# Performance work log

Measured on AMD Instinct MI355X. Metric: run time of the kernel, lower is better.

The kernel has to match this reference:

```python
import jax, jax.numpy as jnp
import numpy as np

D_K = 64
N_HEADS = 16
D_MODEL = 1024


def setup_inputs() -> dict:
    key = jax.random.key(0)
    ks = jax.random.split(key, 12)
    N, T = 2, 2048
    H = D_K * N_HEADS
    s = 1.0 / np.sqrt(D_MODEL)
    inp = {
        "q": jax.random.normal(ks[0], (N, T, D_MODEL), jnp.float32),
        "k": jax.random.normal(ks[1], (N, T, D_MODEL), jnp.float32),
        "v": jax.random.normal(ks[2], (N, T, D_MODEL), jnp.float32),
        "mask": jax.random.randint(ks[3], (N, T), 0, 2, jnp.int32),
        "Wq": jax.random.normal(ks[4], (D_MODEL, H), jnp.float32) * s,
        "bq": jax.random.normal(ks[5], (H,), jnp.float32) * 0.02,
        "Wk": jax.random.normal(ks[6], (D_MODEL, H), jnp.float32) * s,
        "bk": jax.random.normal(ks[7], (H,), jnp.float32) * 0.02,
        "Wv": jax.random.normal(ks[8], (D_MODEL, H), jnp.float32) * s,
        "bv": jax.random.normal(ks[9], (H,), jnp.float32) * 0.02,
        "Wo": jax.random.normal(ks[10], (H, D_MODEL), jnp.float32) * (1.0 / np.sqrt(H)),
        "bo": jax.random.normal(ks[11], (D_MODEL,), jnp.float32) * 0.02,
    }
    return inp


def reference(q, k, v, mask, Wq, bq, Wk, bk, Wv, bv, Wo, bo):
    N, T, _ = q.shape
    # project and split heads: [N, T, H*dk] -> [N, nH, T, dk]
    def split(x):
        return x.reshape(N, T, N_HEADS, D_K).transpose(0, 2, 1, 3)
    qh = split(q @ Wq + bq)
    kh = split(k @ Wk + bk)
    vh = split(v @ Wv + bv)
    scores = jnp.einsum("bhqd,bhkd->bhqk", qh, kh) / np.sqrt(D_K)
    # key padding mask: mask[:, None, None, :] == 0 -> -inf
    scores = jnp.where(mask[:, None, None, :] == 0, -jnp.inf, scores)
    attn = jax.nn.softmax(scores, axis=-1)
    A = jnp.einsum("bhqk,bhkd->bhqd", attn, vh)
    A = A.transpose(0, 2, 1, 3).reshape(N, T, N_HEADS * D_K)
    return A @ Wo + bo
```

## Files before the change

kernel.cpp:

```cpp
#include <hip/hip_runtime.h>

#define T_SEQ 2048
#define DM 1024
#define NH 16
#define DKH 64
#define NB 2
#define M_ROWS (NB * T_SEQ)
#define QSCALE 0.18033688011112042f

using bf16x8 = __attribute__((ext_vector_type(8))) __bf16;
using f32x4  = __attribute__((ext_vector_type(4))) float;
using halfx4 = __attribute__((ext_vector_type(4))) __fp16;
using halfx8 = __attribute__((ext_vector_type(8))) __fp16;
using halfx2 = __attribute__((ext_vector_type(2))) __fp16;
using uintx4 = __attribute__((ext_vector_type(4))) unsigned;

__device__ __forceinline__ short f2bf(float f) {
  unsigned u = __builtin_bit_cast(unsigned, f);
  u += 0x7fffu + ((u >> 16) & 1u);
  return (short)(u >> 16);
}

#if defined(__has_builtin) && __has_builtin(__builtin_amdgcn_cvt_pk_bf16_f32)
using bf16x2 = __attribute__((ext_vector_type(2))) __bf16;
__device__ __forceinline__ short2 pk2(float a, float b) {
  bf16x2 r = __builtin_amdgcn_cvt_pk_bf16_f32(a, b);
  return __builtin_bit_cast(short2, r);
}
#else
__device__ __forceinline__ short2 pk2(float a, float b) {
  short2 r; r.x = f2bf(a); r.y = f2bf(b); return r;
}
#endif

__device__ __forceinline__ short2 pkh(float a, float b) {
  halfx2 r = __builtin_amdgcn_cvt_pkrtz(a, b);
  return __builtin_bit_cast(short2, r);
}

#if defined(__has_builtin) && __has_builtin(__builtin_amdgcn_exp2f)
__device__ __forceinline__ float fexp2(float x) { return __builtin_amdgcn_exp2f(x); }
#else
__device__ __forceinline__ float fexp2(float x) { return exp2f(x); }
#endif

#if defined(__has_builtin) && __has_builtin(__builtin_amdgcn_permlane32_swap) && \
    __has_builtin(__builtin_amdgcn_permlane16_swap)
using uintx2 = __attribute__((ext_vector_type(2))) unsigned;
__device__ __forceinline__ void swap32(unsigned& a, unsigned& b) {
  uintx2 r = __builtin_amdgcn_permlane32_swap(a, b, false, false);
  a = r.x; b = r.y;
}
__device__ __forceinline__ void swap16(unsigned& a, unsigned& b) {
  uintx2 r = __builtin_amdgcn_permlane16_swap(a, b, false, false);
  a = r.x; b = r.y;
}
#else
__device__ __forceinline__ void swap32(unsigned& a, unsigned& b) {
  asm volatile("v_permlane32_swap_b32 %0, %1" : "+v"(a), "+v"(b));
}
__device__ __forceinline__ void swap16(unsigned& a, unsigned& b) {
  asm volatile("v_permlane16_swap_b32 %0, %1" : "+v"(a), "+v"(b));
}
#endif

#define GLD16(g, l)                                                            \
  __builtin_amdgcn_global_load_lds(                                            \
      (const __attribute__((address_space(1))) void*)(g),                      \
      (__attribute__((address_space(3))) void*)(l), 16, 0, 0)

__global__ __launch_bounds__(256) void prep_x(
    const float* __restrict__ q, const float* __restrict__ k,
    const float* __restrict__ v, const int* __restrict__ mask,
    short* __restrict__ dst, float* __restrict__ mf) {
  const float* s = blockIdx.z == 0 ? q : (blockIdx.z == 1 ? k : v);
  short* d = dst + (size_t)blockIdx.z * (M_ROWS * DM);
  const int n4 = M_ROWS * DM / 4;
  for (int i = blockIdx.x * 256 + threadIdx.x; i < n4; i += gridDim.x * 256) {
    float4 f = *(const float4*)(s + i * 4);
    short2 a = pk2(f.x, f.y), b = pk2(f.z, f.w);
    short4 o = {a.x, a.y, b.x, b.y};
    *(short4*)(d + i * 4) = o;
  }
  if (blockIdx.z == 0 && blockIdx.x < 4) {
    int i = (blockIdx.x * 256 + threadIdx.x) * 4;
    int4 m = *(const int4*)(mask + i);
    float4 o = {m.x ? 0.f : -1e38f, m.y ? 0.f : -1e38f,
                m.z ? 0.f : -1e38f, m.w ? 0.f : -1e38f};
    *(float4*)(mf + i) = o;
  }
}

__global__ __launch_bounds__(256) void prep_w(
    const float* __restrict__ w0, const float* __restrict__ w1,
    const float* __restrict__ w2, const float* __restrict__ w3,
    short* __restrict__ dst) {
  __shared__ short T[64][72];
  const float* W = blockIdx.z == 0 ? w0 : blockIdx.z == 1 ? w1
                   : blockIdx.z == 2 ? w2 : w3;
  short* D = dst + (size_t)blockIdx.z * (DM * DM);
  const int k0 = blockIdx.x * 64, n0 = blockIdx.y * 64;
  const int r = threadIdx.x >> 2, cs = (threadIdx.x & 3) * 16;
#pragma unroll
  for (int j = 0; j < 4; ++j) {
    float4 f = *(const float4*)(W + (size_t)(k0 + r) * DM + n0 + cs + j * 4);
    short2 a = pk2(f.x, f.y), b = pk2(f.z, f.w);
    short4 o = {a.x, a.y, b.x, b.y};
    *(short4*)&T[r][cs + j * 4] = o;
  }
  __syncthreads();
  short tmp[16];
#pragma unroll
  for (int i = 0; i < 16; ++i) tmp[i] = T[cs + i][r];
  *(int4*)(D + (size_t)(n0 + r) * DM + k0 + cs) = *(const int4*)&tmp[0];
  *(int4*)(D + (size_t)(n0 + r) * DM + k0 + cs + 8) = *(const int4*)&tmp[8];
}

__global__ __launch_bounds__(512) void gemm_qkv(
    const short* __restrict__ A_, const short* __restrict__ Bt_,
    const float* __restrict__ b0, const float* __restrict__ b1,
    const float* __restrict__ b2, short* __restrict__ Y) {
  __shared__ short As[2][4096];
  __shared__ short Bs[2][4096];
  const int z = blockIdx.z;
  const short* A = A_ + (size_t)z * (M_ROWS * DM);
  const short* Bt = Bt_ + (size_t)z * (DM * DM);
  short* Yz = Y + (size_t)z * ((size_t)M_ROWS * DM);
  const float* bias = z == 0 ? b0 : (z == 1 ? b1 : b2);
  const int m0 = blockIdx.x * 128, n0 = blockIdx.y * 128;
  const int tid = threadIdx.x, w = tid >> 6, lane = tid & 63;
  const int quad = lane >> 4, lm = lane & 15, wa = w & 1, wb = w >> 1;

  const short* Ag = A + (size_t)(m0 + w * 16 + lm) * DM + quad * 8;
  const short* Bg = Bt + (size_t)(n0 + w * 16 + lm) * DM + quad * 8;

  f32x4 acc[4][2];
#pragma unroll
  for (int i = 0; i < 4; ++i)
#pragma unroll
    for (int j = 0; j < 2; ++j) acc[i][j] = (f32x4){0.f, 0.f, 0.f, 0.f};

  GLD16(Ag, &As[0][w * 512]);
  GLD16(Bg, &Bs[0][w * 512]);

  for (int kt = 0; kt < DM / 32; ++kt) {
    const int cb = kt & 1;
    __syncthreads();
    if (kt + 1 < DM / 32) {
      GLD16(Ag + (kt + 1) * 32, &As[cb ^ 1][w * 512]);
      GLD16(Bg + (kt + 1) * 32, &Bs[cb ^ 1][w * 512]);
    }
    bf16x8 af[4], bfr[2];
#pragma unroll
    for (int i = 0; i < 4; ++i)
      af[i] = *(const bf16x8*)&As[cb][(wa * 4 + i) * 512 + quad * 128 + lm * 8];
#pragma unroll
    for (int j = 0; j < 2; ++j)
      bfr[j] = *(const bf16x8*)&Bs[cb][(wb * 2 + j) * 512 + quad * 128 + lm * 8];
#pragma unroll
    for (int mi = 0; mi < 4; ++mi)
#pragma unroll
      for (int j = 0; j < 2; ++j)
        acc[mi][j] = __builtin_amdgcn_mfma_f32_16x16x32_bf16(
            af[mi], bfr[j], acc[mi][j], 0, 0, 0);
  }

  if (z < 2) {
#pragma unroll
    for (int j = 0; j < 2; ++j) {
      const int f = n0 + (wb * 2 + j) * 16 + lm;
      const float bv = bias[f];
      const int h = f >> 6, dk = f & 63;
#pragma unroll
      for (int mi = 0; mi < 4; ++mi)
#pragma unroll
        for (int r = 0; r < 4; ++r) {
          const int m = m0 + (wa * 4 + mi) * 16 + quad * 4 + r;
          float val = acc[mi][j][r] + bv;
          if (z == 0) val *= QSCALE;
          const int b = m >> 11, tt = m & (T_SEQ - 1);
          Yz[(((size_t)(b * NH + h) << 11) + tt) * DKH + dk] = f2bf(val);
        }
    }
  } else {
#pragma unroll
    for (int j = 0; j < 2; ++j) {
      const int f = n0 + (wb * 2 + j) * 16 + lm;
      const float bv = bias[f];
      const int h = f >> 6, dk = f & 63;
#pragma unroll
      for (int mi = 0; mi < 4; ++mi) {
        const int t = m0 + (wa * 4 + mi) * 16 + quad * 4;
        const int b = t >> 11, tt = t & (T_SEQ - 1);
        short2 a = pkh(acc[mi][j][0] + bv, acc[mi][j][1] + bv);
        short2 c = pkh(acc[mi][j][2] + bv, acc[mi][j][3] + bv);
        short4 o = {a.x, a.y, c.x, c.y};
        *(short4*)(Yz + (((size_t)(b * NH + h) * DKH + dk) << 11) + tt) = o;
      }
    }
  }
}

__global__ __launch_bounds__(512) void gemm_out(
    const short* __restrict__ A, const short* __restrict__ Bt,
    const float* __restrict__ bias, float* __restrict__ Yf) {
  __shared__ short As[2][4096];
  __shared__ short Bs[2][2048];
  const int m0 = blockIdx.x * 128, n0 = blockIdx.y * 64;
  const int tid = threadIdx.x, w = tid >> 6, lane = tid & 63;
  const int quad = lane >> 4, lm = lane & 15, wa = w & 3, wb = w >> 2;

  const short* Ag = A + (size_t)(m0 + w * 16 + lm) * DM + quad * 8;
  const short* Bg = Bt + (size_t)(n0 + (w & 3) * 16 + lm) * DM + quad * 8;

  f32x4 acc[2][2];
#pragma unroll
  for (int i = 0; i < 2; ++i)
#pragma unroll
    for (int j = 0; j < 2; ++j) acc[i][j] = (f32x4){0.f, 0.f, 0.f, 0.f};

  GLD16(Ag, &As[0][w * 512]);
  if (w < 4) GLD16(Bg, &Bs[0][w * 512]);

  for (int kt = 0; kt < DM / 32; ++kt) {
    const int cb = kt & 1;
    __syncthreads();
    if (kt + 1 < DM / 32) {
      GLD16(Ag + (kt + 1) * 32, &As[cb ^ 1][w * 512]);
      if (w < 4) GLD16(Bg + (kt + 1) * 32, &Bs[cb ^ 1][w * 512]);
    }
    bf16x8 af[2], bfr[2];
#pragma unroll
    for (int i = 0; i < 2; ++i)
      af[i] = *(const bf16x8*)&As[cb][(wa * 2 + i) * 512 + quad * 128 + lm * 8];
#pragma unroll
    for (int j = 0; j < 2; ++j)
      bfr[j] = *(const bf16x8*)&Bs[cb][(wb * 2 + j) * 512 + quad * 128 + lm * 8];
#pragma unroll
    for (int mi = 0; mi < 2; ++mi)
#pragma unroll
      for (int j = 0; j < 2; ++j)
        acc[mi][j] = __builtin_amdgcn_mfma_f32_16x16x32_bf16(
            af[mi], bfr[j], acc[mi][j], 0, 0, 0);
  }

#pragma unroll
  for (int j = 0; j < 2; ++j) {
    const int n = n0 + (wb * 2 + j) * 16 + lm;
    const float bv = bias[n];
#pragma unroll
    for (int mi = 0; mi < 2; ++mi)
#pragma unroll
      for (int r = 0; r < 4; ++r) {
        const int m = m0 + (wa * 2 + mi) * 16 + quad * 4 + r;
        Yf[(size_t)m * DM + n] = acc[mi][j][r] + bv;
      }
  }
}

__global__ __launch_bounds__(512) void attn_kernel(
    const short* __restrict__ Qh, const short* __restrict__ Kh,
    const short* __restrict__ Vt, const float* __restrict__ mf,
    short* __restrict__ Ao) {
  __shared__ short Ks[2][8192];
  __shared__ short Vs[2][8192];
  const int id = blockIdx.x + gridDim.x * blockIdx.y;
  const int bh = id & 31, qt = id >> 5;
  const int b = bh >> 4, h = bh & (NH - 1);
  const int tid = threadIdx.x, w = tid >> 6, lane = tid & 63;
  const int quad = lane >> 4, lm = lane & 15;
  const size_t base = (size_t)bh * T_SEQ * DKH;
  const float* mp = mf + b * T_SEQ;
  const int q0 = qt * 256 + w * 32;

  const short* qpA = Qh + base + (size_t)(q0 + lm) * DKH;
  const short* qpB = qpA + (size_t)16 * DKH;
  const bf16x8 qbA0 = *(const bf16x8*)(qpA + quad * 8);
  const bf16x8 qbA1 = *(const bf16x8*)(qpA + 32 + quad * 8);
  const bf16x8 qbB0 = *(const bf16x8*)(qpB + quad * 8);
  const bf16x8 qbB1 = *(const bf16x8*)(qpB + 32 + quad * 8);

  const int sw = w & 3;
  const bool isV = w >= 4;
  const short* Kg = Kh + base + (size_t)(sw * 16 + lm) * DKH + quad * 8;
  const short* Vg = Vt + base + (size_t)(sw * 16 + lm) * T_SEQ + quad * 8;

  f32x4 otA[4], otB[4];
#pragma unroll
  for (int i = 0; i < 4; ++i) {
    otA[i] = (f32x4){0.f, 0.f, 0.f, 0.f};
    otB[i] = (f32x4){0.f, 0.f, 0.f, 0.f};
  }
  float lA = 0.f, lB = 0.f;

  if (!isV) {
    GLD16(Kg, &Ks[0][sw * 1024]);
    GLD16(Kg + 32, &Ks[0][sw * 1024 + 512]);
    GLD16(Kg + (size_t)64 * DKH, &Ks[0][(sw + 4) * 1024]);
    GLD16(Kg + (size_t)64 * DKH + 32, &Ks[0][(sw + 4) * 1024 + 512]);
  } else {
    GLD16(Vg, &Vs[0][sw * 2048]);
    GLD16(Vg + 32, &Vs[0][sw * 2048 + 512]);
    GLD16(Vg + 64, &Vs[0][sw * 2048 + 1024]);
    GLD16(Vg + 96, &Vs[0][sw * 2048 + 1536]);
  }

  for (int kt = 0; kt < T_SEQ / 128; ++kt) {
    const int cb = kt & 1;
    const int key0 = kt * 128;
    __syncthreads();
    if (kt + 1 < T_SEQ / 128) {
      const int nk = key0 + 128;
      if (!isV) {
        GLD16(Kg + (size_t)nk * DKH, &Ks[cb ^ 1][sw * 1024]);
        GLD16(Kg + (size_t)nk * DKH + 32, &Ks[cb ^ 1][sw * 1024 + 512]);
        GLD16(Kg + (size_t)(nk + 64) * DKH, &Ks[cb ^ 1][(sw + 4) * 1024]);
        GLD16(Kg + (size_t)(nk + 64) * DKH + 32, &Ks[cb ^ 1][(sw + 4) * 1024 + 512]);
      } else {
        GLD16(Vg + nk, &Vs[cb ^ 1][sw * 2048]);
        GLD16(Vg + nk + 32, &Vs[cb ^ 1][sw * 2048 + 512]);
        GLD16(Vg + nk + 64, &Vs[cb ^ 1][sw * 2048 + 1024]);
        GLD16(Vg + nk + 96, &Vs[cb ^ 1][sw * 2048 + 1536]);
      }
    }

    halfx8 pbA[4], pbB[4];
#pragma unroll
    for (int kp = 0; kp < 4; ++kp) {
      unsigned peA0, peA1, poA0, poA1;
      unsigned peB0, peB1, poB0, poB1;
#pragma unroll
      for (int hf = 0; hf < 2; ++hf) {
        const int nt = kp * 2 + hf;
        bf16x8 ka0 = *(const bf16x8*)&Ks[cb][nt * 1024 + quad * 128 + lm * 8];
        bf16x8 ka1 = *(const bf16x8*)&Ks[cb][nt * 1024 + 512 + quad * 128 + lm * 8];
        f32x4 sA = (f32x4){0.f, 0.f, 0.f, 0.f};
        sA = __builtin_amdgcn_mfma_f32_16x16x32_bf16(ka0, qbA0, sA, 0, 0, 0);
        sA = __builtin_amdgcn_mfma_f32_16x16x32_bf16(ka1, qbA1, sA, 0, 0, 0);
        f32x4 sB = (f32x4){0.f, 0.f, 0.f, 0.f};
        sB = __builtin_amdgcn_mfma_f32_16x16x32_bf16(ka0, qbB0, sB, 0, 0, 0);
        sB = __builtin_amdgcn_mfma_f32_16x16x32_bf16(ka1, qbB1, sB, 0, 0, 0);
        const float4 m4 = *(const float4*)(mp + key0 + nt * 16 + quad * 4);
        float a0 = fexp2(sA[0] + m4.x);
        float a1 = fexp2(sA[1] + m4.y);
        float a2 = fexp2(sA[2] + m4.z);
        float a3 = fexp2(sA[3] + m4.w);
        lA += (a0 + a1) + (a2 + a3);
        float b0 = fexp2(sB[0] + m4.x);
        float b1 = fexp2(sB[1] + m4.y);
        float b2 = fexp2(sB[2] + m4.z);
        float b3 = fexp2(sB[3] + m4.w);
        lB += (b0 + b1) + (b2 + b3);
        unsigned loA = __builtin_bit_cast(unsigned, pkh(a0, a1));
        unsigned hiA = __builtin_bit_cast(unsigned, pkh(a2, a3));
        unsigned loB = __builtin_bit_cast(unsigned, pkh(b0, b1));
        unsigned hiB = __builtin_bit_cast(unsigned, pkh(b2, b3));
        if (hf == 0) {
          peA0 = loA; peA1 = hiA; peB0 = loB; peB1 = hiB;
        } else {
          poA0 = loA; poA1 = hiA; poB0 = loB; poB1 = hiB;
        }
      }
      {
        unsigned x0 = peA0, y0 = poA0, x1 = peA1, y1 = poA1;
        swap32(x0, y0); swap16(x0, y0);
        swap32(x1, y1); swap16(x1, y1);
        pbA[kp] = __builtin_bit_cast(halfx8, (uintx4){x0, x1, y0, y1});
      }
      {
        unsigned x0 = peB0, y0 = poB0, x1 = peB1, y1 = poB1;
        swap32(x0, y0); swap16(x0, y0);
        swap32(x1, y1); swap16(x1, y1);
        pbB[kp] = __builtin_bit_cast(halfx8, (uintx4){x0, x1, y0, y1});
      }
    }

#pragma unroll
    for (int nt2 = 0; nt2 < 4; ++nt2) {
#pragma unroll
      for (int kp = 0; kp < 4; ++kp) {
        halfx8 va =
            *(const halfx8*)&Vs[cb][nt2 * 2048 + kp * 512 + quad * 128 + lm * 8];
        otA[nt2] =
            __builtin_amdgcn_mfma_f32_16x16x32_f16(va, pbA[kp], otA[nt2], 0, 0, 0);
        otB[nt2] =
            __builtin_amdgcn_mfma_f32_16x16x32_f16(va, pbB[kp], otB[nt2], 0, 0, 0);
      }
    }
  }
  lA += __shfl_xor(lA, 16, 64);
  lA += __shfl_xor(lA, 32, 64);
  lB += __shfl_xor(lB, 16, 64);
  lB += __shfl_xor(lB, 32, 64);
  const float invA = 1.f / lA;
  const float invB = 1.f / lB;
  const size_t rowA = (size_t)(b * T_SEQ + q0 + lm) * DM + h * DKH;
  const size_t rowB = rowA + (size_t)16 * DM;
#pragma unroll
  for (int nt = 0; nt < 4; ++nt) {
    short2 a = pk2(otA[nt][0] * invA, otA[nt][1] * invA);
    short2 c = pk2(otA[nt][2] * invA, otA[nt][3] * invA);
    short4 o4 = {a.x, a.y, c.x, c.y};
    *(short4*)(Ao + rowA + nt * 16 + quad * 4) = o4;
    short2 e = pk2(otB[nt][0] * invB, otB[nt][1] * invB);
    short2 g = pk2(otB[nt][2] * invB, otB[nt][3] * invB);
    short4 o5 = {e.x, e.y, g.x, g.y};
    *(short4*)(Ao + rowB + nt * 16 + quad * 4) = o5;
  }
}

extern "C" void kernel_launch(void* const* d_in, const int* in_sizes, int n_in,
                              void* d_out, int out_size, void* d_ws, size_t ws_size,
                              hipStream_t stream) {
  const float* q = (const float*)d_in[0];
  const float* k = (const float*)d_in[1];
  const float* v = (const float*)d_in[2];
  const int* mk = (const int*)d_in[3];
  const float* Wq = (const float*)d_in[4];
  const float* bq = (const float*)d_in[5];
  const float* Wk = (const float*)d_in[6];
  const float* bk = (const float*)d_in[7];
  const float* Wv = (const float*)d_in[8];
  const float* bv = (const float*)d_in[9];
  const float* Wo = (const float*)d_in[10];
  const float* bo = (const float*)d_in[11];

  const size_t XE = (size_t)M_ROWS * DM;
  const size_t WE = (size_t)DM * DM;
  short* xb = (short*)d_ws;
  short* Wt = xb + 3 * XE;
  short* Qh = Wt + 4 * WE;
  float* mf = (float*)(Qh + 3 * XE);
  short* Ao = xb;

  prep_x<<<dim3(1024, 1, 3), 256, 0, stream>>>(q, k, v, mk, xb, mf);
  prep_w<<<dim3(16, 16, 4), 256, 0, stream>>>(Wq, Wk, Wv, Wo, Wt);
  gemm_qkv<<<dim3(M_ROWS / 128, DM / 128, 3), 512, 0, stream>>>(
      xb, Wt, bq, bk, bv, Qh);
  attn_kernel<<<dim3(T_SEQ / 256, NB * NH), 512, 0, stream>>>(
      Qh, Qh + XE, Qh + 2 * XE, mf, Ao);
  gemm_out<<<dim3(M_ROWS / 128, DM / 64), 512, 0, stream>>>(
      Ao, Wt + 3 * WE, bo, (float*)d_out);
}
```

Baseline: 254.2 us.

## Shrink attention blocks to 128 queries with 4 waves each loading K and V

The attention kernel now launches 256-thread blocks covering 128 query rows instead of 512-thread blocks covering 256, doubling the grid to 512 blocks. Each of the four waves now loads both a K slice and a V slice per tile, instead of splitting waves into K-loaders and V-loaders. This improves CU coverage and lets more blocks co-reside. The cost is that each K/V tile is reused by half as many queries, so global and LDS load traffic per query doubles.

```diff
diff --git a/kernel.cpp b/kernel.cpp
--- a/kernel.cpp
+++ b/kernel.cpp
@@ -258,7 +258,7 @@
   }
 }
 
-__global__ __launch_bounds__(512) void attn_kernel(
+__global__ __launch_bounds__(256) void attn_kernel(
     const short* __restrict__ Qh, const short* __restrict__ Kh,
     const short* __restrict__ Vt, const float* __restrict__ mf,
     short* __restrict__ Ao) {
@@ -271,7 +271,7 @@
   const int quad = lane >> 4, lm = lane & 15;
   const size_t base = (size_t)bh * T_SEQ * DKH;
   const float* mp = mf + b * T_SEQ;
-  const int q0 = qt * 256 + w * 32;
+  const int q0 = qt * 128 + w * 32;
 
   const short* qpA = Qh + base + (size_t)(q0 + lm) * DKH;
   const short* qpB = qpA + (size_t)16 * DKH;
@@ -280,10 +280,8 @@
   const bf16x8 qbB0 = *(const bf16x8*)(qpB + quad * 8);
   const bf16x8 qbB1 = *(const bf16x8*)(qpB + 32 + quad * 8);
 
-  const int sw = w & 3;
-  const bool isV = w >= 4;
-  const short* Kg = Kh + base + (size_t)(sw * 16 + lm) * DKH + quad * 8;
-  const short* Vg = Vt + base + (size_t)(sw * 16 + lm) * T_SEQ + quad * 8;
+  const short* Kg = Kh + base + (size_t)(w * 16 + lm) * DKH + quad * 8;
+  const short* Vg = Vt + base + (size_t)(w * 16 + lm) * T_SEQ + quad * 8;
 
   f32x4 otA[4], otB[4];
 #pragma unroll
@@ -293,17 +291,14 @@
   }
   float lA = 0.f, lB = 0.f;
 
-  if (!isV) {
-    GLD16(Kg, &Ks[0][sw * 1024]);
-    GLD16(Kg + 32, &Ks[0][sw * 1024 + 512]);
-    GLD16(Kg + (size_t)64 * DKH, &Ks[0][(sw + 4) * 1024]);
-    GLD16(Kg + (size_t)64 * DKH + 32, &Ks[0][(sw + 4) * 1024 + 512]);
-  } else {
-    GLD16(Vg, &Vs[0][sw * 2048]);
-    GLD16(Vg + 32, &Vs[0][sw * 2048 + 512]);
-    GLD16(Vg + 64, &Vs[0][sw * 2048 + 1024]);
-    GLD16(Vg + 96, &Vs[0][sw * 2048 + 1536]);
-  }
+  GLD16(Kg, &Ks[0][w * 1024]);
+  GLD16(Kg + 32, &Ks[0][w * 1024 + 512]);
+  GLD16(Kg + (size_t)64 * DKH, &Ks[0][(w + 4) * 1024]);
+  GLD16(Kg + (size_t)64 * DKH + 32, &Ks[0][(w + 4) * 1024 + 512]);
+  GLD16(Vg, &Vs[0][w * 2048]);
+  GLD16(Vg + 32, &Vs[0][w * 2048 + 512]);
+  GLD16(Vg + 64, &Vs[0][w * 2048 + 1024]);
+  GLD16(Vg + 96, &Vs[0][w * 2048 + 1536]);
 
   for (int kt = 0; kt < T_SEQ / 128; ++kt) {
     const int cb = kt & 1;
@@ -311,17 +306,14 @@
     __syncthreads();
     if (kt + 1 < T_SEQ / 128) {
       const int nk = key0 + 128;
-      if (!isV) {
-        GLD16(Kg + (size_t)nk * DKH, &Ks[cb ^ 1][sw * 1024]);
-        GLD16(Kg + (size_t)nk * DKH + 32, &Ks[cb ^ 1][sw * 1024 + 512]);
-        GLD16(Kg + (size_t)(nk + 64) * DKH, &Ks[cb ^ 1][(sw + 4) * 1024]);
-        GLD16(Kg + (size_t)(nk + 64) * DKH + 32, &Ks[cb ^ 1][(sw + 4) * 1024 + 512]);
-      } else {
-        GLD16(Vg + nk, &Vs[cb ^ 1][sw * 2048]);
-        GLD16(Vg + nk + 32, &Vs[cb ^ 1][sw * 2048 + 512]);
-        GLD16(Vg + nk + 64, &Vs[cb ^ 1][sw * 2048 + 1024]);
-        GLD16(Vg + nk + 96, &Vs[cb ^ 1][sw * 2048 + 1536]);
-      }
+      GLD16(Kg + (size_t)nk * DKH, &Ks[cb ^ 1][w * 1024]);
+      GLD16(Kg + (size_t)nk * DKH + 32, &Ks[cb ^ 1][w * 1024 + 512]);
+      GLD16(Kg + (size_t)(nk + 64) * DKH, &Ks[cb ^ 1][(w + 4) * 1024]);
+      GLD16(Kg + (size_t)(nk + 64) * DKH + 32, &Ks[cb ^ 1][(w + 4) * 1024 + 512]);
+      GLD16(Vg + nk, &Vs[cb ^ 1][w * 2048]);
+      GLD16(Vg + nk + 32, &Vs[cb ^ 1][w * 2048 + 512]);
+      GLD16(Vg + nk + 64, &Vs[cb ^ 1][w * 2048 + 1024]);
+      GLD16(Vg + nk + 96, &Vs[cb ^ 1][w * 2048 + 1536]);
     }
 
     halfx8 pbA[4], pbB[4];
@@ -437,7 +429,7 @@
   prep_w<<<dim3(16, 16, 4), 256, 0, stream>>>(Wq, Wk, Wv, Wo, Wt);
   gemm_qkv<<<dim3(M_ROWS / 128, DM / 128, 3), 512, 0, stream>>>(
       xb, Wt, bq, bk, bv, Qh);
-  attn_kernel<<<dim3(T_SEQ / 256, NB * NH), 512, 0, stream>>>(
+  attn_kernel<<<dim3(T_SEQ / 128, NB * NH), 256, 0, stream>>>(
       Qh, Qh + XE, Qh + 2 * XE, mf, Ao);
   gemm_out<<<dim3(M_ROWS / 128, DM / 64), 512, 0, stream>>>(
       Ao, Wt + 3 * WE, bo, (float*)d_out);
```

Measured after the change: 272.8 us. 1.07x slower.

## Fuse fp32-to-bf16 activation conversion into QKV GEMM and swap grid order

Applied to the files above, without the earlier changes.

Removes the separate prep_x pass that converted q/k/v to bf16 in a workspace. The QKV GEMM now reads fp32 activations directly, converts them in registers and stores the bf16 tile to LDS, with the next tile's loads issued before the barrier. Both GEMM grids are also reordered so blocks sharing an M tile run together, which is meant to improve L2 reuse of the activation rows. The trade-off is that the GEMM now moves twice the A bytes and uses register-staged loads in place of direct global-to-LDS copies.

```diff
diff --git a/kernel.cpp b/kernel.cpp
--- a/kernel.cpp
+++ b/kernel.cpp
@@ -69,26 +69,13 @@
       (const __attribute__((address_space(1))) void*)(g),                      \
       (__attribute__((address_space(3))) void*)(l), 16, 0, 0)
 
-__global__ __launch_bounds__(256) void prep_x(
-    const float* __restrict__ q, const float* __restrict__ k,
-    const float* __restrict__ v, const int* __restrict__ mask,
-    short* __restrict__ dst, float* __restrict__ mf) {
-  const float* s = blockIdx.z == 0 ? q : (blockIdx.z == 1 ? k : v);
-  short* d = dst + (size_t)blockIdx.z * (M_ROWS * DM);
-  const int n4 = M_ROWS * DM / 4;
-  for (int i = blockIdx.x * 256 + threadIdx.x; i < n4; i += gridDim.x * 256) {
-    float4 f = *(const float4*)(s + i * 4);
-    short2 a = pk2(f.x, f.y), b = pk2(f.z, f.w);
-    short4 o = {a.x, a.y, b.x, b.y};
-    *(short4*)(d + i * 4) = o;
-  }
-  if (blockIdx.z == 0 && blockIdx.x < 4) {
-    int i = (blockIdx.x * 256 + threadIdx.x) * 4;
-    int4 m = *(const int4*)(mask + i);
-    float4 o = {m.x ? 0.f : -1e38f, m.y ? 0.f : -1e38f,
-                m.z ? 0.f : -1e38f, m.w ? 0.f : -1e38f};
-    *(float4*)(mf + i) = o;
-  }
+__global__ __launch_bounds__(256) void prep_mask(
+    const int* __restrict__ mask, float* __restrict__ mf) {
+  int i = (blockIdx.x * 256 + threadIdx.x) * 4;
+  int4 m = *(const int4*)(mask + i);
+  float4 o = {m.x ? 0.f : -1e38f, m.y ? 0.f : -1e38f,
+              m.z ? 0.f : -1e38f, m.w ? 0.f : -1e38f};
+  *(float4*)(mf + i) = o;
 }
 
 __global__ __launch_bounds__(256) void prep_w(
@@ -117,22 +104,24 @@
 }
 
 __global__ __launch_bounds__(512) void gemm_qkv(
-    const short* __restrict__ A_, const short* __restrict__ Bt_,
+    const float* __restrict__ q, const float* __restrict__ k,
+    const float* __restrict__ v, const short* __restrict__ Bt_,
     const float* __restrict__ b0, const float* __restrict__ b1,
     const float* __restrict__ b2, short* __restrict__ Y) {
   __shared__ short As[2][4096];
   __shared__ short Bs[2][4096];
   const int z = blockIdx.z;
-  const short* A = A_ + (size_t)z * (M_ROWS * DM);
+  const float* A32 = z == 0 ? q : (z == 1 ? k : v);
   const short* Bt = Bt_ + (size_t)z * (DM * DM);
   short* Yz = Y + (size_t)z * ((size_t)M_ROWS * DM);
   const float* bias = z == 0 ? b0 : (z == 1 ? b1 : b2);
-  const int m0 = blockIdx.x * 128, n0 = blockIdx.y * 128;
+  const int n0 = blockIdx.x * 128, m0 = blockIdx.y * 128;
   const int tid = threadIdx.x, w = tid >> 6, lane = tid & 63;
   const int quad = lane >> 4, lm = lane & 15, wa = w & 1, wb = w >> 1;
 
-  const short* Ag = A + (size_t)(m0 + w * 16 + lm) * DM + quad * 8;
+  const float* Ag = A32 + (size_t)(m0 + w * 16 + lm) * DM + quad * 8;
   const short* Bg = Bt + (size_t)(n0 + w * 16 + lm) * DM + quad * 8;
+  short* Ad = &As[0][w * 512 + quad * 128 + lm * 8];
 
   f32x4 acc[4][2];
 #pragma unroll
@@ -140,15 +129,33 @@
 #pragma unroll
     for (int j = 0; j < 2; ++j) acc[i][j] = (f32x4){0.f, 0.f, 0.f, 0.f};
 
-  GLD16(Ag, &As[0][w * 512]);
+  {
+    float4 fa = *(const float4*)(Ag);
+    float4 fb = *(const float4*)(Ag + 4);
+    int4 o = {__builtin_bit_cast(int, pk2(fa.x, fa.y)),
+              __builtin_bit_cast(int, pk2(fa.z, fa.w)),
+              __builtin_bit_cast(int, pk2(fb.x, fb.y)),
+              __builtin_bit_cast(int, pk2(fb.z, fb.w))};
+    *(int4*)Ad = o;
+  }
   GLD16(Bg, &Bs[0][w * 512]);
 
   for (int kt = 0; kt < DM / 32; ++kt) {
     const int cb = kt & 1;
+    float4 fa, fb;
+    const bool more = kt + 1 < DM / 32;
+    if (more) {
+      fa = *(const float4*)(Ag + (kt + 1) * 32);
+      fb = *(const float4*)(Ag + (kt + 1) * 32 + 4);
+    }
     __syncthreads();
-    if (kt + 1 < DM / 32) {
-      GLD16(Ag + (kt + 1) * 32, &As[cb ^ 1][w * 512]);
+    if (more) {
       GLD16(Bg + (kt + 1) * 32, &Bs[cb ^ 1][w * 512]);
+      int4 o = {__builtin_bit_cast(int, pk2(fa.x, fa.y)),
+                __builtin_bit_cast(int, pk2(fa.z, fa.w)),
+                __builtin_bit_cast(int, pk2(fb.x, fb.y)),
+                __builtin_bit_cast(int, pk2(fb.z, fb.w))};
+      *(int4*)(Ad + (cb ^ 1) * 4096) = o;
     }
     bf16x8 af[4], bfr[2];
 #pragma unroll
@@ -206,7 +213,7 @@
     const float* __restrict__ bias, float* __restrict__ Yf) {
   __shared__ short As[2][4096];
   __shared__ short Bs[2][2048];
-  const int m0 = blockIdx.x * 128, n0 = blockIdx.y * 64;
+  const int n0 = blockIdx.x * 64, m0 = blockIdx.y * 128;
   const int tid = threadIdx.x, w = tid >> 6, lane = tid & 63;
   const int quad = lane >> 4, lm = lane & 15, wa = w & 3, wb = w >> 2;
 
@@ -433,12 +440,12 @@
   float* mf = (float*)(Qh + 3 * XE);
   short* Ao = xb;
 
-  prep_x<<<dim3(1024, 1, 3), 256, 0, stream>>>(q, k, v, mk, xb, mf);
+  prep_mask<<<dim3(4, 1, 1), 256, 0, stream>>>(mk, mf);
   prep_w<<<dim3(16, 16, 4), 256, 0, stream>>>(Wq, Wk, Wv, Wo, Wt);
-  gemm_qkv<<<dim3(M_ROWS / 128, DM / 128, 3), 512, 0, stream>>>(
-      xb, Wt, bq, bk, bv, Qh);
+  gemm_qkv<<<dim3(DM / 128, M_ROWS / 128, 3), 512, 0, stream>>>(
+      q, k, v, Wt, bq, bk, bv, Qh);
   attn_kernel<<<dim3(T_SEQ / 256, NB * NH), 512, 0, stream>>>(
       Qh, Qh + XE, Qh + 2 * XE, mf, Ao);
-  gemm_out<<<dim3(M_ROWS / 128, DM / 64), 512, 0, stream>>>(
+  gemm_out<<<dim3(DM / 64, M_ROWS / 128), 512, 0, stream>>>(
       Ao, Wt + 3 * WE, bo, (float*)d_out);
 }
```

Result: slower. 273.3 us (+7.5%).

## Merge prep kernels and load GEMM B fragments directly from global memory

Applied to the files above, without the earlier changes.

Combines the activation cast and weight transpose/cast into one launch using a z-split grid, removing one kernel launch. In both GEMMs, B-operand fragments are now read straight from global memory into registers each k-step instead of being staged through double-buffered LDS. This frees LDS and cuts LDS traffic, but the per-wave global loads are redundant across waves and exposed in latency, since they are issued right before use with no prefetch.

```diff
diff --git a/kernel.cpp b/kernel.cpp
--- a/kernel.cpp
+++ b/kernel.cpp
@@ -69,36 +69,38 @@
       (const __attribute__((address_space(1))) void*)(g),                      \
       (__attribute__((address_space(3))) void*)(l), 16, 0, 0)
 
-__global__ __launch_bounds__(256) void prep_x(
+__global__ __launch_bounds__(256) void prep_all(
     const float* __restrict__ q, const float* __restrict__ k,
     const float* __restrict__ v, const int* __restrict__ mask,
-    short* __restrict__ dst, float* __restrict__ mf) {
-  const float* s = blockIdx.z == 0 ? q : (blockIdx.z == 1 ? k : v);
-  short* d = dst + (size_t)blockIdx.z * (M_ROWS * DM);
-  const int n4 = M_ROWS * DM / 4;
-  for (int i = blockIdx.x * 256 + threadIdx.x; i < n4; i += gridDim.x * 256) {
-    float4 f = *(const float4*)(s + i * 4);
-    short2 a = pk2(f.x, f.y), b = pk2(f.z, f.w);
-    short4 o = {a.x, a.y, b.x, b.y};
-    *(short4*)(d + i * 4) = o;
-  }
-  if (blockIdx.z == 0 && blockIdx.x < 4) {
-    int i = (blockIdx.x * 256 + threadIdx.x) * 4;
-    int4 m = *(const int4*)(mask + i);
-    float4 o = {m.x ? 0.f : -1e38f, m.y ? 0.f : -1e38f,
-                m.z ? 0.f : -1e38f, m.w ? 0.f : -1e38f};
-    *(float4*)(mf + i) = o;
-  }
-}
-
-__global__ __launch_bounds__(256) void prep_w(
     const float* __restrict__ w0, const float* __restrict__ w1,
     const float* __restrict__ w2, const float* __restrict__ w3,
-    short* __restrict__ dst) {
+    short* __restrict__ dst, short* __restrict__ wdst,
+    float* __restrict__ mf) {
+  const int z = blockIdx.z;
+  if (z < 3) {
+    const float* s = z == 0 ? q : (z == 1 ? k : v);
+    short* d = dst + (size_t)z * (M_ROWS * DM);
+    const int bid = blockIdx.y * 16 + blockIdx.x;
+    const int n4 = M_ROWS * DM / 4;
+    for (int i = bid * 256 + threadIdx.x; i < n4; i += 256 * 256) {
+      float4 f = *(const float4*)(s + i * 4);
+      short2 a = pk2(f.x, f.y), b = pk2(f.z, f.w);
+      short4 o = {a.x, a.y, b.x, b.y};
+      *(short4*)(d + i * 4) = o;
+    }
+    if (z == 0 && bid < 4) {
+      int i = (bid * 256 + threadIdx.x) * 4;
+      int4 m = *(const int4*)(mask + i);
+      float4 o = {m.x ? 0.f : -1e38f, m.y ? 0.f : -1e38f,
+                  m.z ? 0.f : -1e38f, m.w ? 0.f : -1e38f};
+      *(float4*)(mf + i) = o;
+    }
+    return;
+  }
   __shared__ short T[64][72];
-  const float* W = blockIdx.z == 0 ? w0 : blockIdx.z == 1 ? w1
-                   : blockIdx.z == 2 ? w2 : w3;
-  short* D = dst + (size_t)blockIdx.z * (DM * DM);
+  const int wz = z - 3;
+  const float* W = wz == 0 ? w0 : wz == 1 ? w1 : wz == 2 ? w2 : w3;
+  short* D = wdst + (size_t)wz * (DM * DM);
   const int k0 = blockIdx.x * 64, n0 = blockIdx.y * 64;
   const int r = threadIdx.x >> 2, cs = (threadIdx.x & 3) * 16;
 #pragma unroll
@@ -121,7 +123,6 @@
     const float* __restrict__ b0, const float* __restrict__ b1,
     const float* __restrict__ b2, short* __restrict__ Y) {
   __shared__ short As[2][4096];
-  __shared__ short Bs[2][4096];
   const int z = blockIdx.z;
   const short* A = A_ + (size_t)z * (M_ROWS * DM);
   const short* Bt = Bt_ + (size_t)z * (DM * DM);
@@ -132,7 +133,8 @@
   const int quad = lane >> 4, lm = lane & 15, wa = w & 1, wb = w >> 1;
 
   const short* Ag = A + (size_t)(m0 + w * 16 + lm) * DM + quad * 8;
-  const short* Bg = Bt + (size_t)(n0 + w * 16 + lm) * DM + quad * 8;
+  const short* Bg0 = Bt + (size_t)(n0 + (wb * 2) * 16 + lm) * DM + quad * 8;
+  const short* Bg1 = Bg0 + (size_t)16 * DM;
 
   f32x4 acc[4][2];
 #pragma unroll
@@ -141,22 +143,20 @@
     for (int j = 0; j < 2; ++j) acc[i][j] = (f32x4){0.f, 0.f, 0.f, 0.f};
 
   GLD16(Ag, &As[0][w * 512]);
-  GLD16(Bg, &Bs[0][w * 512]);
 
   for (int kt = 0; kt < DM / 32; ++kt) {
     const int cb = kt & 1;
+    bf16x8 bfr[2];
+    bfr[0] = *(const bf16x8*)(Bg0 + kt * 32);
+    bfr[1] = *(const bf16x8*)(Bg1 + kt * 32);
     __syncthreads();
     if (kt + 1 < DM / 32) {
       GLD16(Ag + (kt + 1) * 32, &As[cb ^ 1][w * 512]);
-      GLD16(Bg + (kt + 1) * 32, &Bs[cb ^ 1][w * 512]);
-    }
-    bf16x8 af[4], bfr[2];
+    }
+    bf16x8 af[4];
 #pragma unroll
     for (int i = 0; i < 4; ++i)
       af[i] = *(const bf16x8*)&As[cb][(wa * 4 + i) * 512 + quad * 128 + lm * 8];
-#pragma unroll
-    for (int j = 0; j < 2; ++j)
-      bfr[j] = *(const bf16x8*)&Bs[cb][(wb * 2 + j) * 512 + quad * 128 + lm * 8];
 #pragma unroll
     for (int mi = 0; mi < 4; ++mi)
 #pragma unroll
@@ -205,13 +205,13 @@
     const short* __restrict__ A, const short* __restrict__ Bt,
     const float* __restrict__ bias, float* __restrict__ Yf) {
   __shared__ short As[2][4096];
-  __shared__ short Bs[2][2048];
   const int m0 = blockIdx.x * 128, n0 = blockIdx.y * 64;
   const int tid = threadIdx.x, w = tid >> 6, lane = tid & 63;
   const int quad = lane >> 4, lm = lane & 15, wa = w & 3, wb = w >> 2;
 
   const short* Ag = A + (size_t)(m0 + w * 16 + lm) * DM + quad * 8;
-  const short* Bg = Bt + (size_t)(n0 + (w & 3) * 16 + lm) * DM + quad * 8;
+  const short* Bg0 = Bt + (size_t)(n0 + (wb * 2) * 16 + lm) * DM + quad * 8;
+  const short* Bg1 = Bg0 + (size_t)16 * DM;
 
   f32x4 acc[2][2];
 #pragma unroll
@@ -220,22 +220,20 @@
     for (int j = 0; j < 2; ++j) acc[i][j] = (f32x4){0.f, 0.f, 0.f, 0.f};
 
   GLD16(Ag, &As[0][w * 512]);
-  if (w < 4) GLD16(Bg, &Bs[0][w * 512]);
 
   for (int kt = 0; kt < DM / 32; ++kt) {
     const int cb = kt & 1;
+    bf16x8 bfr[2];
+    bfr[0] = *(const bf16x8*)(Bg0 + kt * 32);
+    bfr[1] = *(const bf16x8*)(Bg1 + kt * 32);
     __syncthreads();
     if (kt + 1 < DM / 32) {
       GLD16(Ag + (kt + 1) * 32, &As[cb ^ 1][w * 512]);
-      if (w < 4) GLD16(Bg + (kt + 1) * 32, &Bs[cb ^ 1][w * 512]);
-    }
-    bf16x8 af[2], bfr[2];
+    }
+    bf16x8 af[2];
 #pragma unroll
     for (int i = 0; i < 2; ++i)
       af[i] = *(const bf16x8*)&As[cb][(wa * 2 + i) * 512 + quad * 128 + lm * 8];
-#pragma unroll
-    for (int j = 0; j < 2; ++j)
-      bfr[j] = *(const bf16x8*)&Bs[cb][(wb * 2 + j) * 512 + quad * 128 + lm * 8];
 #pragma unroll
     for (int mi = 0; mi < 2; ++mi)
 #pragma unroll
@@ -433,8 +431,8 @@
   float* mf = (float*)(Qh + 3 * XE);
   short* Ao = xb;
 
-  prep_x<<<dim3(1024, 1, 3), 256, 0, stream>>>(q, k, v, mk, xb, mf);
-  prep_w<<<dim3(16, 16, 4), 256, 0, stream>>>(Wq, Wk, Wv, Wo, Wt);
+  prep_all<<<dim3(16, 16, 7), 256, 0, stream>>>(q, k, v, mk, Wq, Wk, Wv, Wo,
+                                                xb, Wt, mf);
   gemm_qkv<<<dim3(M_ROWS / 128, DM / 128, 3), 512, 0, stream>>>(
       xb, Wt, bq, bk, bv, Qh);
   attn_kernel<<<dim3(T_SEQ / 256, NB * NH), 512, 0, stream>>>(
```

Measured after the change: 295.0 us. 1.16x slower.
